# Kernel optimization log

Measured on AMD Instinct MI355X. Metric: run time of the kernel, lower is better.

The kernel has to match this reference:

```python
import jax, jax.numpy as jnp
import numpy as np

B, N, DEG = 16, 1723, 8   # batch, mesh vertices, avg degree
C, L = 512, 5             # num_channels, num_layers


def _gn(x, g, b, G):
    # GroupNorm over (B, C, N), normalize per group over (C//G, N)
    Bx, Cx, Nx = x.shape
    xr = x.reshape(Bx, G, Cx // G, Nx)
    m = xr.mean(axis=(2, 3), keepdims=True)
    v = xr.var(axis=(2, 3), keepdims=True)
    xr = (xr - m) * jax.lax.rsqrt(v + 1e-5)
    return xr.reshape(Bx, Cx, Nx) * g[None, :, None] + b[None, :, None]


def _glin(W, b, x):
    # per-vertex linear: (O,I) @ (B,I,N) + b
    return jnp.einsum('oi,bin->bon', W, x) + b[None, :, None]


def _gconv(x, W, b, src, dst, w):
    # GraphConvolution: support = x^T @ W, then sparse adjacency spmm via edge list
    sup = jnp.einsum('bcn,cd->bnd', x, W)          # (B, N, C)
    msg = sup[:, src, :] * w[None, :, None]        # gather neighbors (B, E, C)
    agg = jnp.zeros_like(sup).at[:, dst, :].add(msg) + b[None, None, :]
    return agg.transpose(0, 2, 1)                  # back to (B, C, N)


def _resblock(x, p, src, dst, w):
    (pre_g, pre_b, l1W, l1b, n1g, n1b, cW, cb, n2g, n2b, l2W, l2b, skW, skb) = p
    Cin, Ch = x.shape[1], l1W.shape[0]
    y = jax.nn.relu(_gn(x, pre_g, pre_b, Cin // 8))
    y = _glin(l1W, l1b, y)
    y = jax.nn.relu(_gn(y, n1g, n1b, Ch // 8))
    y = _gconv(y, cW, cb, src, dst, w)
    y = jax.nn.relu(_gn(y, n2g, n2b, Ch // 8))
    y = _glin(l2W, l2b, y)
    if skW is not None:
        x = _glin(skW, skb, x)
    return x + y


def setup_inputs() -> dict:
    key = jax.random.key(0)
    ks = iter(jax.random.split(key, 64))
    s = 0.02
    w = lambda shp: jax.random.normal(next(ks), shp, jnp.float32) * s
    z = lambda shp: jnp.zeros(shp, jnp.float32)
    o = lambda shp: jnp.ones(shp, jnp.float32)
    H = C // 2
    E = N * DEG
    inp = {}
    inp['image_resnet'] = jax.random.normal(next(ks), (B, 2048), jnp.float32)
    inp['ref_vertices'] = jax.random.normal(next(ks), (3, N), jnp.float32)
    inp['adj_src'] = jax.random.randint(next(ks), (E,), 0, N, jnp.int32)
    inp['adj_dst'] = jnp.repeat(jnp.arange(N, dtype=jnp.int32), DEG)
    inp['adj_w'] = jnp.full((E,), 1.0 / DEG, jnp.float32)
    inp['lin0_W'] = w((2 * C, 3 + 2048)); inp['lin0_b'] = z((2 * C,))
    inp['b0_pre_g'] = o((2 * C,)); inp['b0_pre_b'] = z((2 * C,))
    inp['b0_lin1_W'] = w((H, 2 * C)); inp['b0_lin1_b'] = z((H,))
    inp['b0_n1_g'] = o((H,)); inp['b0_n1_b'] = z((H,))
    inp['b0_conv_W'] = w((H, H)); inp['b0_conv_b'] = z((H,))
    inp['b0_n2_g'] = o((H,)); inp['b0_n2_b'] = z((H,))
    inp['b0_lin2_W'] = w((C, H)); inp['b0_lin2_b'] = z((C,))
    inp['b0_skip_W'] = w((C, 2 * C)); inp['b0_skip_b'] = z((C,))
    inp['blk_pre_g'] = o((L, C)); inp['blk_pre_b'] = z((L, C))
    inp['blk_lin1_W'] = w((L, H, C)); inp['blk_lin1_b'] = z((L, H))
    inp['blk_n1_g'] = o((L, H)); inp['blk_n1_b'] = z((L, H))
    inp['blk_conv_W'] = w((L, H, H)); inp['blk_conv_b'] = z((L, H))
    inp['blk_n2_g'] = o((L, H)); inp['blk_n2_b'] = z((L, H))
    inp['blk_lin2_W'] = w((L, C, H)); inp['blk_lin2_b'] = z((L, C))
    inp['h1_W'] = w((64, C)); inp['h1_b'] = z((64,))
    inp['h2_W'] = w((32, 64)); inp['h2_b'] = z((32,))
    inp['hn_g'] = o((32,)); inp['hn_b'] = z((32,))
    inp['h3_W'] = w((3, 32)); inp['h3_b'] = z((3,))
    return inp


def reference(image_resnet, ref_vertices, adj_src, adj_dst, adj_w,
              lin0_W, lin0_b,
              b0_pre_g, b0_pre_b, b0_lin1_W, b0_lin1_b, b0_n1_g, b0_n1_b,
              b0_conv_W, b0_conv_b, b0_n2_g, b0_n2_b, b0_lin2_W, b0_lin2_b,
              b0_skip_W, b0_skip_b,
              blk_pre_g, blk_pre_b, blk_lin1_W, blk_lin1_b, blk_n1_g, blk_n1_b,
              blk_conv_W, blk_conv_b, blk_n2_g, blk_n2_b, blk_lin2_W, blk_lin2_b,
              h1_W, h1_b, h2_W, h2_b, hn_g, hn_b, h3_W, h3_b):
    Bx, Nv = image_resnet.shape[0], ref_vertices.shape[1]
    img = jnp.broadcast_to(image_resnet[:, :, None], (Bx, 2048, Nv))
    verts = jnp.broadcast_to(ref_vertices[None], (Bx, 3, Nv))
    x = jnp.concatenate([verts, img], axis=1)                 # (B, 2051, N)
    x = _glin(lin0_W, lin0_b, x)                              # (B, 1024, N)
    x = _resblock(x, (b0_pre_g, b0_pre_b, b0_lin1_W, b0_lin1_b, b0_n1_g, b0_n1_b,
                      b0_conv_W, b0_conv_b, b0_n2_g, b0_n2_b, b0_lin2_W, b0_lin2_b,
                      b0_skip_W, b0_skip_b), adj_src, adj_dst, adj_w)  # (B, 512, N)
    for i in range(blk_pre_g.shape[0]):
        x = _resblock(x, (blk_pre_g[i], blk_pre_b[i], blk_lin1_W[i], blk_lin1_b[i],
                          blk_n1_g[i], blk_n1_b[i], blk_conv_W[i], blk_conv_b[i],
                          blk_n2_g[i], blk_n2_b[i], blk_lin2_W[i], blk_lin2_b[i],
                          None, None), adj_src, adj_dst, adj_w)
    # shape decoder head
    y = jax.nn.relu(_glin(h1_W, h1_b, x))
    y = _glin(h2_W, h2_b, y)
    y = jax.nn.relu(_gn(y, hn_g, hn_b, 4))   # GroupNorm(32//8, 32)
    y = _glin(h3_W, h3_b, y)                 # (B, 3, N)
    return y
```

## Files before the change

### kernel.cpp

```cpp
#include <hip/hip_runtime.h>
#include <cstddef>
#include <cstdint>

#define THREADS 256

typedef short bh8 __attribute__((ext_vector_type(8)));
typedef float fx4 __attribute__((ext_vector_type(4)));

__device__ __forceinline__ float bf2f(unsigned short u) {
  union { unsigned int i; float f; } x;
  x.i = ((unsigned int)u) << 16;
  return x.f;
}
__device__ __forceinline__ unsigned short f2bf(float f) {
  union { float f; unsigned int i; } x;
  x.f = f;
  unsigned int r = x.i + 0x7fffu + ((x.i >> 16) & 1u);
  return (unsigned short)(r >> 16);
}

__device__ __forceinline__ void gld16(const void* g, void* l) {
  __builtin_amdgcn_global_load_lds(
      (const __attribute__((address_space(1))) unsigned int*)g,
      (__attribute__((address_space(3))) unsigned int*)l, 16, 0, 0);
}

__global__ __launch_bounds__(THREADS) void transpose_img_k(
    const float* __restrict__ img, float* __restrict__ imgT) {
  int gid = blockIdx.x * THREADS + threadIdx.x;
  if (gid >= 2048 * 16) return;
  int k = gid >> 4, b = gid & 15;
  imgT[k * 16 + b] = img[b * 2048 + k];
}

__global__ __launch_bounds__(THREADS) void pack_wv_k(
    const float* __restrict__ W, float* __restrict__ wv) {
  int gid = blockIdx.x * THREADS + threadIdx.x;
  if (gid >= 3 * 1024) return;
  int k = gid >> 10, c = gid & 1023;
  wv[gid] = W[(size_t)c * 2051 + k];
}

__global__ __launch_bounds__(THREADS) void vertproj_k(
    const float* __restrict__ wv, const float* __restrict__ verts,
    float* __restrict__ v, int N) {
  int gid = blockIdx.x * THREADS + threadIdx.x;
  int c = gid & 1023, n = gid >> 10;
  if (n >= N) return;
  v[(size_t)n * 1024 + c] =
      wv[c] * verts[n] + wv[1024 + c] * verts[N + n] + wv[2048 + c] * verts[2 * N + n];
}

__global__ __launch_bounds__(THREADS) void ugemm2_k(
    const float* __restrict__ W, int ldw, int woff,
    const float* __restrict__ bias, const float* __restrict__ X,
    float* __restrict__ out, int K, int Ofull, int xl, int ks) {
  int tid = threadIdx.x;
  int b = tid & 15, cl = tid >> 4;
  int c = blockIdx.x * 16 + cl;
  int k0 = blockIdx.y * ks, k1 = k0 + ks;
  const float* wr = W + woff + (size_t)c * ldw;
  float a0 = 0.f, a1 = 0.f;
  if (xl) {
    const float* xr = X + (size_t)b * K;
    for (int k = k0; k < k1; k += 2) {
      a0 = fmaf(wr[k], xr[k], a0);
      a1 = fmaf(wr[k + 1], xr[k + 1], a1);
    }
  } else {
    for (int k = k0; k < k1; k += 2) {
      a0 = fmaf(wr[k], X[k * 16 + b], a0);
      a1 = fmaf(wr[k + 1], X[(k + 1) * 16 + b], a1);
    }
  }
  float r = a0 + a1;
  if (blockIdx.y == 0) r += bias[c];
  atomicAdd(&out[(size_t)b * Ofull + c], r);
}

struct PackDesc {
  const float* W;
  unsigned short* out;
  int O, K, TW, nOt;
  unsigned cum;
};
struct PackArgs {
  PackDesc d[8];
  unsigned grand;
};

__global__ __launch_bounds__(THREADS) void packall_k(PackArgs a) {
  unsigned gid = blockIdx.x * THREADS + threadIdx.x;
  if (gid >= a.grand) return;
  int s = 0;
#pragma unroll
  for (int i = 1; i < 8; ++i)
    if (gid >= a.d[i].cum) s = i;
#pragma unroll
  for (int i = 0; i < 8; ++i) {
    if (s != i) continue;
    const float* W = a.d[i].W;
    int O = a.d[i].O, K = a.d[i].K, TW = a.d[i].TW, nOt = a.d[i].nOt;
    unsigned e = gid - a.d[i].cum;
    int j = (int)(e & 7);
    int m = (int)((e >> 3) & 127);
    unsigned rest = e >> 10;
    int K8 = K >> 3;
    int kg = (int)(rest % (unsigned)K8);
    unsigned rest2 = rest / (unsigned)K8;
    int ot = (int)(rest2 % (unsigned)nOt);
    int l = (int)(rest2 / (unsigned)nOt);
    int o = ot * 128 + m, k = kg * 8 + j;
    float val = 0.f;
    if (o < O)
      val = TW ? W[(size_t)l * O * K + (size_t)k * O + o]
               : W[(size_t)l * O * K + (size_t)o * K + k];
    a.d[i].out[e] = f2bf(val);
  }
}

__global__ __launch_bounds__(THREADS) void vstats_k(
    const float* __restrict__ v, float* __restrict__ sv,
    float* __restrict__ sq, int N) {
  int c = blockIdx.x * THREADS + threadIdx.x;
  float s = 0.f, q = 0.f;
  for (int n = blockIdx.y; n < N; n += 16) {
    float x = v[(size_t)n * 1024 + c];
    s += x; q += x * x;
  }
  atomicAdd(&sv[c], s);
  atomicAdd(&sq[c], q);
}

__global__ __launch_bounds__(THREADS) void combine_b0_k(
    const float* __restrict__ ub, const float* __restrict__ sv,
    const float* __restrict__ sq, float* __restrict__ mean,
    float* __restrict__ rinv, int N) {
  int bg = blockIdx.x * THREADS + threadIdx.x;
  if (bg >= 2048) return;
  int b = bg >> 7, g = bg & 127;
  int c0 = g * 8;
  float fN = (float)N;
  float s = 0.f, q = 0.f;
#pragma unroll
  for (int j = 0; j < 8; ++j) {
    float u = ub[b * 1024 + c0 + j];
    float svc = sv[c0 + j];
    s += fN * u + svc;
    q += fN * u * u + 2.f * u * svc + sq[c0 + j];
  }
  float inv = 1.f / (8.f * fN);
  float m = s * inv;
  float var = q * inv - m * m;
  mean[bg] = m;
  rinv[bg] = rsqrtf(var + 1e-5f);
}

__global__ __launch_bounds__(THREADS) void agg16_k(
    const unsigned short* __restrict__ Xn, const float* __restrict__ sarr,
    const float* __restrict__ qarr, const float* __restrict__ gamma,
    const float* __restrict__ beta, const int* __restrict__ src,
    const float* __restrict__ wgt, unsigned short* __restrict__ outb, int N,
    int NPn) {
  int w = threadIdx.x >> 6, lane = threadIdx.x & 63;
  int n = blockIdx.x * 4 + w;
  if (n >= N) return;
  int b = blockIdx.y;
  int c = lane * 4;
  int g = c >> 3;
  float sfac = 1.f / (8.f * (float)N);
  float svv = sarr[b * 32 + g], qv = qarr[b * 32 + g];
  float m = svv * sfac;
  float ri = rsqrtf(qv * sfac - m * m + 1e-5f);
  float4 g4 = *(const float4*)(gamma + c);
  float4 b4 = *(const float4*)(beta + c);
  const int* sp = src + n * 8;
  const float* wp = wgt + n * 8;
  const unsigned short* base = Xn + (size_t)b * NPn * 256;
  float a0 = 0.f, a1 = 0.f, a2 = 0.f, a3 = 0.f;
#pragma unroll
  for (int j = 0; j < 8; ++j) {
    int sidx = sp[j];
    float wj = wp[j];
    ushort4 x4 = *(const ushort4*)(base + (size_t)sidx * 256 + c);
    a0 = fmaf(wj, fmaxf((bf2f(x4.x) - m) * ri * g4.x + b4.x, 0.f), a0);
    a1 = fmaf(wj, fmaxf((bf2f(x4.y) - m) * ri * g4.y + b4.y, 0.f), a1);
    a2 = fmaf(wj, fmaxf((bf2f(x4.z) - m) * ri * g4.z + b4.z, 0.f), a2);
    a3 = fmaf(wj, fmaxf((bf2f(x4.w) - m) * ri * g4.w + b4.w, 0.f), a3);
  }
  ushort4 h;
  h.x = f2bf(a0); h.y = f2bf(a1); h.z = f2bf(a2); h.w = f2bf(a3);
  *(ushort4*)(outb + ((size_t)b * NPn + n) * 256 + c) = h;
}

template <int XM, int RES, int OUT16, int ORELU, int STATS>
__global__ __launch_bounds__(THREADS) void mgemm_k(
    const unsigned short* __restrict__ Wp, const float* __restrict__ bias,
    const void* __restrict__ Xv, const float* __restrict__ ub,
    const float* __restrict__ vv, const float* __restrict__ meanS,
    const float* __restrict__ rinvS, const float* __restrict__ gamma,
    const float* __restrict__ beta, const float* __restrict__ resA,
    const float* __restrict__ resB, float* __restrict__ sacc,
    float* __restrict__ qacc, void* __restrict__ outv, int O, int I, int N,
    int NPn) {
  constexpr int BBUF = (XM == 4) ? 2 : 1;
  __shared__ unsigned short Alds[2][4][128][8];
  __shared__ unsigned short Blds[BBUF][4][128][8];
  const int tid = threadIdx.x;
  const int lane = tid & 63;
  const int wid = tid >> 6;
  const int wm = wid & 1, wn = wid >> 1;
  const int n0 = blockIdx.x * 128;
  const int o0 = blockIdx.y * 128;
  const int b = blockIdx.z;
  const int K8 = I >> 3;
  const unsigned short* wp = Wp + (size_t)blockIdx.y * K8 * 1024;

  fx4 acc[4][4];
#pragma unroll
  for (int i = 0; i < 4; ++i)
#pragma unroll
    for (int j = 0; j < 4; ++j) {
      acc[i][j][0] = 0.f; acc[i][j][1] = 0.f;
      acc[i][j][2] = 0.f; acc[i][j][3] = 0.f;
    }

  const int sko = tid >> 6;
  const int sn = (tid & 63) * 2;
  const int mlane = lane & 15;
  const int klane = lane >> 4;

  auto dmaA = [&](int k0, int buf) {
    const unsigned short* asrc = wp + (size_t)(k0 >> 3) * 1024;
    unsigned short* ab = &Alds[buf][0][0][0];
    gld16(asrc + (size_t)tid * 8, ab + (size_t)tid * 8);
    gld16(asrc + (size_t)(tid + 256) * 8, ab + (size_t)(tid + 256) * 8);
  };
  auto dmaB4 = [&](int k0, int buf) {
    const unsigned short* xs =
        (const unsigned short*)Xv + ((size_t)b * NPn + n0) * I + k0 + wid * 8;
    unsigned short* bb = &Blds[buf][0][0][0] + (size_t)wid * 1024;
    gld16(xs + (size_t)lane * I, bb + (size_t)lane * 8);
    gld16(xs + (size_t)(lane + 64) * I, bb + 512 + (size_t)lane * 8);
  };

  uint4 br0, br1;
  float4 f00, f01, f10, f11, u01, u23;

  auto gloadB = [&](int k0) {
    const int ke = k0 + sko * 8;
    if (XM == 3) {
      const unsigned short* p =
          (const unsigned short*)Xv + ((size_t)b * NPn + n0 + sn) * I + ke;
      br0 = *(const uint4*)p;
      br1 = *(const uint4*)(p + I);
    } else if (XM == 1) {
      const float* p = vv + (size_t)(n0 + sn) * I + ke;
      f00 = *(const float4*)p;       f01 = *(const float4*)(p + 4);
      f10 = *(const float4*)(p + I); f11 = *(const float4*)(p + I + 4);
      const float* up = ub + (size_t)b * I + ke;
      u01 = *(const float4*)up;
      u23 = *(const float4*)(up + 4);
    } else if (XM == 0 || XM == 2) {
      const float* p = (const float*)Xv + ((size_t)b * NPn + n0 + sn) * I + ke;
      f00 = *(const float4*)p;       f01 = *(const float4*)(p + 4);
      f10 = *(const float4*)(p + I); f11 = *(const float4*)(p + I + 4);
    }
  };

  union H8 { unsigned short u[8]; uint4 q; };

  auto bstoreB = [&](int k0) {
    const int ke = k0 + sko * 8;
    float x0[8], x1[8];
    if (XM == 3) {
      H8 hr0, hr1;
      hr0.q = br0; hr1.q = br1;
#pragma unroll
      for (int j = 0; j < 8; ++j) {
        x0[j] = bf2f(hr0.u[j]);
        x1[j] = bf2f(hr1.u[j]);
      }
    } else {
      x0[0] = f00.x; x0[1] = f00.y; x0[2] = f00.z; x0[3] = f00.w;
      x0[4] = f01.x; x0[5] = f01.y; x0[6] = f01.z; x0[7] = f01.w;
      x1[0] = f10.x; x1[1] = f10.y; x1[2] = f10.z; x1[3] = f10.w;
      x1[4] = f11.x; x1[5] = f11.y; x1[6] = f11.z; x1[7] = f11.w;
    }
    if (XM == 1) {
      float uu[8] = {u01.x, u01.y, u01.z, u01.w, u23.x, u23.y, u23.z, u23.w};
#pragma unroll
      for (int j = 0; j < 8; ++j) { x0[j] += uu[j]; x1[j] += uu[j]; }
    }
    if (XM != 0) {
      float m_, r_;
      if (XM == 1) {
        m_ = meanS[b * K8 + (ke >> 3)];
        r_ = rinvS[b * K8 + (ke >> 3)];
      } else {
        float sfac = 1.f / (8.f * (float)N);
        float sv = meanS[b * K8 + (ke >> 3)];
        float qv = rinvS[b * K8 + (ke >> 3)];
        m_ = sv * sfac;
        r_ = rsqrtf(qv * sfac - m_ * m_ + 1e-5f);
      }
      float4 g0 = *(const float4*)(gamma + ke);
      float4 g1 = *(const float4*)(gamma + ke + 4);
      float4 e0 = *(const float4*)(beta + ke);
      float4 e1 = *(const float4*)(beta + ke + 4);
      float ga[8] = {g0.x, g0.y, g0.z, g0.w, g1.x, g1.y, g1.z, g1.w};
      float bb[8] = {e0.x, e0.y, e0.z, e0.w, e1.x, e1.y, e1.z, e1.w};
#pragma unroll
      for (int j = 0; j < 8; ++j) {
        x0[j] = fmaxf((x0[j] - m_) * r_ * ga[j] + bb[j], 0.f);
        x1[j] = fmaxf((x1[j] - m_) * r_ * ga[j] + bb[j], 0.f);
      }
    }
    H8 h0, h1;
#pragma unroll
    for (int j = 0; j < 8; ++j) {
      h0.u[j] = f2bf(x0[j]);
      h1.u[j] = f2bf(x1[j]);
    }
    *(uint4*)&Blds[0][sko][sn][0] = h0.q;
    *(uint4*)&Blds[0][sko][sn + 1][0] = h1.q;
  };

  auto compute = [&](int ab, int bb) {
    bh8 af[4], bfr[4];
#pragma unroll
    for (int mi = 0; mi < 4; ++mi)
      af[mi] = *(const bh8*)(&Alds[ab][klane][wm * 64 + mi * 16 + mlane][0]);
#pragma unroll
    for (int ni = 0; ni < 4; ++ni)
      bfr[ni] = *(const bh8*)(&Blds[bb][klane][wn * 64 + ni * 16 + mlane][0]);
#pragma unroll
    for (int mi = 0; mi < 4; ++mi)
#pragma unroll
      for (int ni = 0; ni < 4; ++ni)
        acc[mi][ni] = __builtin_amdgcn_mfma_f32_16x16x32_bf16(
            af[mi], bfr[ni], acc[mi][ni], 0, 0, 0);
  };

  if (XM == 4) {
    dmaA(0, 0);
    dmaB4(0, 0);
    __syncthreads();
    for (int k0 = 0; k0 < I; k0 += 32) {
      const int cur = (k0 >> 5) & 1;
      if (k0 + 32 < I) {
        dmaA(k0 + 32, cur ^ 1);
        dmaB4(k0 + 32, cur ^ 1);
      }
      compute(cur, cur);
      __syncthreads();
    }
  } else {
    dmaA(0, 0);
    gloadB(0);
    for (int k0 = 0; k0 < I; k0 += 32) {
      const int cur = (k0 >> 5) & 1;
      bstoreB(k0);
      __syncthreads();
      if (k0 + 32 < I) {
        dmaA(k0 + 32, cur ^ 1);
        gloadB(k0 + 32);
      }
      compute(cur, 0);
      __syncthreads();
    }
  }

  float sred[4] = {0.f, 0.f, 0.f, 0.f};
  float qred[4] = {0.f, 0.f, 0.f, 0.f};
#pragma unroll
  for (int mi = 0; mi < 4; ++mi) {
    const int o = o0 + wm * 64 + mi * 16 + klane * 4;
    if (o >= O) continue;
    float4 bi;
    if (bias) bi = *(const float4*)(bias + o);
    float4 ra;
    if (RES == 2) ra = *(const float4*)(resA + (size_t)b * O + o);
#pragma unroll
    for (int ni = 0; ni < 4; ++ni) {
      const int n = n0 + wn * 64 + ni * 16 + mlane;
      if (n >= N) continue;
      float v0 = acc[mi][ni][0], v1 = acc[mi][ni][1];
      float v2 = acc[mi][ni][2], v3 = acc[mi][ni][3];
      if (bias) { v0 += bi.x; v1 += bi.y; v2 += bi.z; v3 += bi.w; }
      size_t obase = ((size_t)b * NPn + n) * O + o;
      if (RES == 1) {
        float4 rv = *(const float4*)(resA + obase);
        v0 += rv.x; v1 += rv.y; v2 += rv.z; v3 += rv.w;
      }
      if (RES == 2) {
        float4 rb = *(const float4*)(resB + (size_t)n * O + o);
        v0 += ra.x + rb.x; v1 += ra.y + rb.y;
        v2 += ra.z + rb.z; v3 += ra.w + rb.w;
      }
      if (ORELU) {
        v0 = fmaxf(v0, 0.f); v1 = fmaxf(v1, 0.f);
        v2 = fmaxf(v2, 0.f); v3 = fmaxf(v3, 0.f);
      }
      if (STATS) {
        sred[mi] += v0 + v1 + v2 + v3;
        qred[mi] += v0 * v0 + v1 * v1 + v2 * v2 + v3 * v3;
      }
      if (OUT16) {
        ushort4 h;
        h.x = f2bf(v0); h.y = f2bf(v1); h.z = f2bf(v2); h.w = f2bf(v3);
        *(ushort4*)((unsigned short*)outv + obase) = h;
      } else {
        float4 fv; fv.x = v0; fv.y = v1; fv.z = v2; fv.w = v3;
        *(float4*)((float*)outv + obase) = fv;
      }
    }
  }
  if (STATS) {
    const int G = O >> 3;
#pragma unroll
    for (int mi = 0; mi < 4; ++mi) {
      const int o = o0 + wm * 64 + mi * 16 + klane * 4;
      if (o >= O) continue;
      float s = sred[mi], q = qred[mi];
#pragma unroll
      for (int m = 1; m < 16; m <<= 1) {
        s += __shfl_xor(s, m, 64);
        q += __shfl_xor(q, m, 64);
      }
      if (mlane == 0) {
        atomicAdd(&sacc[b * G + (o >> 3)], s);
        atomicAdd(&qacc[b * G + (o >> 3)], q);
      }
    }
  }
}

__global__ __launch_bounds__(THREADS) void h2_k(
    const float* __restrict__ t64, const float* __restrict__ W,
    const float* __restrict__ bias, float* __restrict__ out, int N, int NPn) {
  int gid = blockIdx.x * THREADS + threadIdx.x;
  int o = gid & 31, n = gid >> 5;
  if (n >= N) return;
  int b = blockIdx.y;
  const float* xr = t64 + ((size_t)b * NPn + n) * 64;
  const float* wr = W + o * 64;
  float acc = bias[o];
#pragma unroll
  for (int i = 0; i < 64; i += 4) {
    float4 w4 = *(const float4*)(wr + i);
    float4 x4 = *(const float4*)(xr + i);
    acc += w4.x * x4.x + w4.y * x4.y + w4.z * x4.z + w4.w * x4.w;
  }
  out[((size_t)b * NPn + n) * 32 + o] = acc;
}

__global__ __launch_bounds__(THREADS) void stats_head_k(
    const float* __restrict__ X, float* __restrict__ mean,
    float* __restrict__ rinv, int NPn, int N) {
  int b = blockIdx.x >> 2, g = blockIdx.x & 3;
  int c = g * 8 + (threadIdx.x & 7);
  float s = 0.f, q = 0.f;
  for (int n = threadIdx.x >> 3; n < N; n += 32) {
    float x = X[((size_t)b * NPn + n) * 32 + c];
    s += x; q += x * x;
  }
#pragma unroll
  for (int off = 32; off; off >>= 1) {
    s += __shfl_down(s, off, 64);
    q += __shfl_down(q, off, 64);
  }
  __shared__ float shs[4], shq[4];
  int wv = threadIdx.x >> 6;
  if ((threadIdx.x & 63) == 0) { shs[wv] = s; shq[wv] = q; }
  __syncthreads();
  if (threadIdx.x == 0) {
    s = shs[0] + shs[1] + shs[2] + shs[3];
    q = shq[0] + shq[1] + shq[2] + shq[3];
    float inv = 1.f / (8.f * (float)N);
    float m = s * inv;
    float var = q * inv - m * m;
    mean[blockIdx.x] = m;
    rinv[blockIdx.x] = rsqrtf(var + 1e-5f);
  }
}

__global__ __launch_bounds__(THREADS) void h3_k(
    const float* __restrict__ t32, const float* __restrict__ mean,
    const float* __restrict__ rinv, const float* __restrict__ g,
    const float* __restrict__ be, const float* __restrict__ W,
    const float* __restrict__ bias, float* __restrict__ out, int N, int NPn) {
  int n = blockIdx.x * THREADS + threadIdx.x;
  if (n >= N) return;
  int b = blockIdx.y;
  const float* xr = t32 + ((size_t)b * NPn + n) * 32;
  float y0 = bias[0], y1 = bias[1], y2 = bias[2];
#pragma unroll
  for (int c = 0; c < 32; ++c) {
    float m = mean[b * 4 + (c >> 3)], ri = rinv[b * 4 + (c >> 3)];
    float x = fmaxf((xr[c] - m) * ri * g[c] + be[c], 0.f);
    y0 = fmaf(W[c], x, y0);
    y1 = fmaf(W[32 + c], x, y1);
    y2 = fmaf(W[64 + c], x, y2);
  }
  out[(size_t)b * 3 * N + n] = y0;
  out[(size_t)b * 3 * N + N + n] = y1;
  out[(size_t)b * 3 * N + 2 * N + n] = y2;
}

extern "C" void kernel_launch(void* const* d_in, const int* in_sizes, int n_in,
                              void* d_out, int out_size, void* d_ws,
                              size_t ws_size, hipStream_t stream) {
  (void)n_in; (void)out_size; (void)ws_size;
  const float* img = (const float*)d_in[0];
  const float* verts = (const float*)d_in[1];
  const int* src = (const int*)d_in[2];
  const float* adjw = (const float*)d_in[4];
  const float* lin0_W = (const float*)d_in[5];
  const float* lin0_b = (const float*)d_in[6];
  const float* b0_pre_g = (const float*)d_in[7];
  const float* b0_pre_b = (const float*)d_in[8];
  const float* b0_lin1_W = (const float*)d_in[9];
  const float* b0_lin1_b = (const float*)d_in[10];
  const float* b0_n1_g = (const float*)d_in[11];
  const float* b0_n1_b = (const float*)d_in[12];
  const float* b0_conv_W = (const float*)d_in[13];
  const float* b0_conv_b = (const float*)d_in[14];
  const float* b0_n2_g = (const float*)d_in[15];
  const float* b0_n2_b = (const float*)d_in[16];
  const float* b0_lin2_W = (const float*)d_in[17];
  const float* b0_lin2_b = (const float*)d_in[18];
  const float* b0_skip_W = (const float*)d_in[19];
  const float* b0_skip_b = (const float*)d_in[20];
  const float* blk_pre_g = (const float*)d_in[21];
  const float* blk_pre_b = (const float*)d_in[22];
  const float* blk_lin1_W = (const float*)d_in[23];
  const float* blk_lin1_b = (const float*)d_in[24];
  const float* blk_n1_g = (const float*)d_in[25];
  const float* blk_n1_b = (const float*)d_in[26];
  const float* blk_conv_W = (const float*)d_in[27];
  const float* blk_conv_b = (const float*)d_in[28];
  const float* blk_n2_g = (const float*)d_in[29];
  const float* blk_n2_b = (const float*)d_in[30];
  const float* blk_lin2_W = (const float*)d_in[31];
  const float* blk_lin2_b = (const float*)d_in[32];
  const float* h1_W = (const float*)d_in[33];
  const float* h1_b = (const float*)d_in[34];
  const float* h2_W = (const float*)d_in[35];
  const float* h2_b = (const float*)d_in[36];
  const float* hn_g = (const float*)d_in[37];
  const float* hn_b = (const float*)d_in[38];
  const float* h3_W = (const float*)d_in[39];
  const float* h3_b = (const float*)d_in[40];

  const int N = in_sizes[1] / 3;
  const int NP = ((N + 127) / 128) * 128;
  const int NT128 = NP / 128;
  const int B = 16;

  char* wsb = (char*)d_ws;
  size_t off = 0;
  auto alloc = [&](size_t nbytes) {
    void* p = wsb + off;
    off += (nbytes + 255) & ~(size_t)255;
    return p;
  };
  float* xbuf = (float*)alloc((size_t)B * NP * 512 * 4);
  unsigned short* t256a = (unsigned short*)alloc((size_t)B * NP * 256 * 2);
  unsigned short* t256b = (unsigned short*)alloc((size_t)B * NP * 256 * 2);
  float* vbuf = (float*)alloc((size_t)NP * 1024 * 4);
  float* svbuf = (float*)alloc((size_t)NP * 512 * 4);
  float* t64 = (float*)alloc((size_t)B * NP * 64 * 4);
  float* t32 = (float*)alloc((size_t)B * NP * 32 * 4);
  float* imgT = (float*)alloc(2048 * 16 * 4);
  float* wv = (float*)alloc(3 * 1024 * 4);
  float* m0 = (float*)alloc(2048 * 4);
  float* r0 = (float*)alloc(2048 * 4);
  float* mh = (float*)alloc(64 * 4);
  float* rh = (float*)alloc(64 * 4);
  float* zerobuf = (float*)alloc((size_t)49152 * 4);
  float* sA = zerobuf;
  float* qA = zerobuf + 11264;
  float* sv = zerobuf + 22528;
  float* sq = zerobuf + 23552;
  float* ub = zerobuf + 24576;
  float* suT = zerobuf + 40960;
  const int off_b0n1 = 0, off_b0n2 = 512;
  auto off_pre = [](int l) { return 1024 + l * 2048; };
  auto off_n1 = [](int l) { return 1024 + l * 2048 + 1024; };
  auto off_n2 = [](int l) { return 1024 + l * 2048 + 1536; };
  unsigned short* pw_b0l1 = (unsigned short*)alloc(262144 * 2);
  unsigned short* pw_b0cv = (unsigned short*)alloc(65536 * 2);
  unsigned short* pw_b0l2 = (unsigned short*)alloc(131072 * 2);
  unsigned short* pw_b0sk = (unsigned short*)alloc(524288 * 2);
  unsigned short* pw_l1 = (unsigned short*)alloc(655360 * 2);
  unsigned short* pw_cv = (unsigned short*)alloc(327680 * 2);
  unsigned short* pw_l2 = (unsigned short*)alloc(655360 * 2);
  unsigned short* pw_h1 = (unsigned short*)alloc(65536 * 2);

  dim3 blk(THREADS);
  auto cdiv = [](size_t a, size_t b) { return (unsigned)((a + b - 1) / b); };

  hipMemsetAsync(zerobuf, 0, (size_t)49152 * 4, stream);

  {
    PackArgs pa;
    unsigned c = 0;
    auto set = [&](int i, const float* W, unsigned short* o, int O, int K,
                   int TW, int nOt, unsigned tot) {
      pa.d[i] = {W, o, O, K, TW, nOt, c};
      c += tot;
    };
    set(0, b0_lin1_W, pw_b0l1, 256, 1024, 0, 2, 262144);
    set(1, b0_conv_W, pw_b0cv, 256, 256, 1, 2, 65536);
    set(2, b0_lin2_W, pw_b0l2, 512, 256, 0, 4, 131072);
    set(3, b0_skip_W, pw_b0sk, 512, 1024, 0, 4, 524288);
    set(4, blk_lin1_W, pw_l1, 256, 512, 0, 2, 655360);
    set(5, blk_conv_W, pw_cv, 256, 256, 1, 2, 327680);
    set(6, blk_lin2_W, pw_l2, 512, 256, 0, 4, 655360);
    set(7, h1_W, pw_h1, 64, 512, 0, 1, 65536);
    pa.grand = c;
    packall_k<<<cdiv(pa.grand, THREADS), blk, 0, stream>>>(pa);
  }

  transpose_img_k<<<cdiv(2048 * 16, THREADS), blk, 0, stream>>>(img, imgT);
  pack_wv_k<<<cdiv(3072, THREADS), blk, 0, stream>>>(lin0_W, wv);
  ugemm2_k<<<dim3(64, 16), blk, 0, stream>>>(lin0_W, 2051, 3, lin0_b, imgT,
                                             ub, 2048, 1024, 0, 128);
  vertproj_k<<<cdiv((size_t)N * 1024, THREADS), blk, 0, stream>>>(wv, verts, vbuf, N);

  const dim3 aggGrid(cdiv(N, 4), 16);

  vstats_k<<<dim3(4, 16), blk, 0, stream>>>(vbuf, sv, sq, N);
  combine_b0_k<<<dim3(8), blk, 0, stream>>>(ub, sv, sq, m0, r0, N);
  mgemm_k<1, 0, 1, 0, 1><<<dim3(NT128, 2, 16), blk, 0, stream>>>(
      pw_b0l1, b0_lin1_b, nullptr, ub, vbuf, m0, r0, b0_pre_g, b0_pre_b,
      nullptr, nullptr, sA + off_b0n1, qA + off_b0n1, t256a, 256, 1024, N, NP);
  ugemm2_k<<<dim3(32, 8), blk, 0, stream>>>(b0_skip_W, 1024, 0, b0_skip_b, ub,
                                            suT, 1024, 512, 1, 128);
  mgemm_k<0, 0, 0, 0, 0><<<dim3(NT128, 4, 1), blk, 0, stream>>>(
      pw_b0sk, nullptr, vbuf, nullptr, nullptr, nullptr, nullptr, nullptr,
      nullptr, nullptr, nullptr, nullptr, nullptr, svbuf, 512, 1024, N, NP);
  agg16_k<<<aggGrid, blk, 0, stream>>>(t256a, sA + off_b0n1, qA + off_b0n1,
                                       b0_n1_g, b0_n1_b, src, adjw, t256b, N, NP);
  mgemm_k<4, 0, 1, 0, 1><<<dim3(NT128, 2, 16), blk, 0, stream>>>(
      pw_b0cv, b0_conv_b, t256b, nullptr, nullptr, nullptr, nullptr, nullptr,
      nullptr, nullptr, nullptr, sA + off_b0n2, qA + off_b0n2, t256a, 256, 256, N, NP);
  mgemm_k<3, 2, 0, 0, 1><<<dim3(NT128, 4, 16), blk, 0, stream>>>(
      pw_b0l2, b0_lin2_b, t256a, nullptr, nullptr, sA + off_b0n2, qA + off_b0n2,
      b0_n2_g, b0_n2_b, suT, svbuf, sA + off_pre(0), qA + off_pre(0), xbuf,
      512, 256, N, NP);

  for (int l = 0; l < 5; ++l) {
    const float* pg = blk_pre_g + l * 512;
    const float* pb = blk_pre_b + l * 512;
    const unsigned short* l1W = pw_l1 + (size_t)l * 131072;
    const float* l1b = blk_lin1_b + l * 256;
    const float* n1g = blk_n1_g + l * 256;
    const float* n1b = blk_n1_b + l * 256;
    const unsigned short* cW = pw_cv + (size_t)l * 65536;
    const float* cb = blk_conv_b + l * 256;
    const float* n2g = blk_n2_g + l * 256;
    const float* n2b = blk_n2_b + l * 256;
    const unsigned short* l2W = pw_l2 + (size_t)l * 131072;
    const float* l2b = blk_lin2_b + l * 512;

    mgemm_k<2, 0, 1, 0, 1><<<dim3(NT128, 2, 16), blk, 0, stream>>>(
        l1W, l1b, xbuf, nullptr, nullptr, sA + off_pre(l), qA + off_pre(l), pg,
        pb, nullptr, nullptr, sA + off_n1(l), qA + off_n1(l), t256a, 256, 512, N, NP);
    agg16_k<<<aggGrid, blk, 0, stream>>>(t256a, sA + off_n1(l), qA + off_n1(l),
                                         n1g, n1b, src, adjw, t256b, N, NP);
    mgemm_k<4, 0, 1, 0, 1><<<dim3(NT128, 2, 16), blk, 0, stream>>>(
        cW, cb, t256b, nullptr, nullptr, nullptr, nullptr, nullptr, nullptr,
        nullptr, nullptr, sA + off_n2(l), qA + off_n2(l), t256a, 256, 256, N, NP);
    if (l < 4) {
      mgemm_k<3, 1, 0, 0, 1><<<dim3(NT128, 4, 16), blk, 0, stream>>>(
          l2W, l2b, t256a, nullptr, nullptr, sA + off_n2(l), qA + off_n2(l),
          n2g, n2b, xbuf, nullptr, sA + off_pre(l + 1), qA + off_pre(l + 1),
          xbuf, 512, 256, N, NP);
    } else {
      mgemm_k<3, 1, 0, 0, 0><<<dim3(NT128, 4, 16), blk, 0, stream>>>(
          l2W, l2b, t256a, nullptr, nullptr, sA + off_n2(l), qA + off_n2(l),
          n2g, n2b, xbuf, nullptr, nullptr, nullptr, xbuf, 512, 256, N, NP);
    }
  }

  mgemm_k<0, 0, 0, 1, 0><<<dim3(NT128, 1, 16), blk, 0, stream>>>(
      pw_h1, h1_b, xbuf, nullptr, nullptr, nullptr, nullptr, nullptr, nullptr,
      nullptr, nullptr, nullptr, nullptr, t64, 64, 512, N, NP);
  h2_k<<<dim3(cdiv((size_t)N * 32, THREADS), 16), blk, 0, stream>>>(
      t64, h2_W, h2_b, t32, N, NP);
  stats_head_k<<<dim3(64), blk, 0, stream>>>(t32, mh, rh, NP, N);
  h3_k<<<dim3(cdiv(N, THREADS), 16), blk, 0, stream>>>(
      t32, mh, rh, hn_g, hn_b, h3_W, h3_b, (float*)d_out, N, NP);
}
```

Baseline: 1.401 ms.

## Fuse neighbor aggregation into conv GEMM B-load and keep bf16 residual copy

Removes the standalone agg16 kernel and folds the GroupNorm+ReLU+weighted 8-neighbor gather into a new XM==5 B-tile loader of the graph-conv GEMM. It saves one launch and one intermediate write/read per block. Separately, the lin2 GEMM now also writes a bf16 copy of the residual stream (DUAL), so the next lin1 GEMM reads bf16 instead of fp32. The cost is more registers and gather latency inside the GEMM's B staging, which may lower occupancy or stall the MFMA pipeline. There is also an extra store and extra memory for the bf16 copy.

```diff
diff --git a/kernel.cpp b/kernel.cpp
--- a/kernel.cpp
+++ b/kernel.cpp
@@ -156,53 +156,17 @@
   rinv[bg] = rsqrtf(var + 1e-5f);
 }
 
-__global__ __launch_bounds__(THREADS) void agg16_k(
-    const unsigned short* __restrict__ Xn, const float* __restrict__ sarr,
-    const float* __restrict__ qarr, const float* __restrict__ gamma,
-    const float* __restrict__ beta, const int* __restrict__ src,
-    const float* __restrict__ wgt, unsigned short* __restrict__ outb, int N,
-    int NPn) {
-  int w = threadIdx.x >> 6, lane = threadIdx.x & 63;
-  int n = blockIdx.x * 4 + w;
-  if (n >= N) return;
-  int b = blockIdx.y;
-  int c = lane * 4;
-  int g = c >> 3;
-  float sfac = 1.f / (8.f * (float)N);
-  float svv = sarr[b * 32 + g], qv = qarr[b * 32 + g];
-  float m = svv * sfac;
-  float ri = rsqrtf(qv * sfac - m * m + 1e-5f);
-  float4 g4 = *(const float4*)(gamma + c);
-  float4 b4 = *(const float4*)(beta + c);
-  const int* sp = src + n * 8;
-  const float* wp = wgt + n * 8;
-  const unsigned short* base = Xn + (size_t)b * NPn * 256;
-  float a0 = 0.f, a1 = 0.f, a2 = 0.f, a3 = 0.f;
-#pragma unroll
-  for (int j = 0; j < 8; ++j) {
-    int sidx = sp[j];
-    float wj = wp[j];
-    ushort4 x4 = *(const ushort4*)(base + (size_t)sidx * 256 + c);
-    a0 = fmaf(wj, fmaxf((bf2f(x4.x) - m) * ri * g4.x + b4.x, 0.f), a0);
-    a1 = fmaf(wj, fmaxf((bf2f(x4.y) - m) * ri * g4.y + b4.y, 0.f), a1);
-    a2 = fmaf(wj, fmaxf((bf2f(x4.z) - m) * ri * g4.z + b4.z, 0.f), a2);
-    a3 = fmaf(wj, fmaxf((bf2f(x4.w) - m) * ri * g4.w + b4.w, 0.f), a3);
-  }
-  ushort4 h;
-  h.x = f2bf(a0); h.y = f2bf(a1); h.z = f2bf(a2); h.w = f2bf(a3);
-  *(ushort4*)(outb + ((size_t)b * NPn + n) * 256 + c) = h;
-}
-
-template <int XM, int RES, int OUT16, int ORELU, int STATS>
+template <int XM, int RES, int OUT16, int ORELU, int STATS, int DUAL>
 __global__ __launch_bounds__(THREADS) void mgemm_k(
     const unsigned short* __restrict__ Wp, const float* __restrict__ bias,
     const void* __restrict__ Xv, const float* __restrict__ ub,
     const float* __restrict__ vv, const float* __restrict__ meanS,
     const float* __restrict__ rinvS, const float* __restrict__ gamma,
     const float* __restrict__ beta, const float* __restrict__ resA,
-    const float* __restrict__ resB, float* __restrict__ sacc,
-    float* __restrict__ qacc, void* __restrict__ outv, int O, int I, int N,
-    int NPn) {
+    const float* __restrict__ resB, const int* __restrict__ srcp,
+    const float* __restrict__ wgtp, float* __restrict__ sacc,
+    float* __restrict__ qacc, void* __restrict__ outv,
+    void* __restrict__ outv2, int O, int I, int N, int NPn) {
   constexpr int BBUF = (XM == 4) ? 2 : 1;
   __shared__ unsigned short Alds[2][4][128][8];
   __shared__ unsigned short Blds[BBUF][4][128][8];
@@ -246,6 +210,24 @@
 
   uint4 br0, br1;
   float4 f00, f01, f10, f11, u01, u23;
+  int go0[8], go1[8];
+  float gw0[8], gw1[8];
+  uint4 g0[8], g1[8];
+  if (XM == 5) {
+    int nc0 = n0 + sn; if (nc0 >= N) nc0 = N - 1;
+    int nc1 = n0 + sn + 1; if (nc1 >= N) nc1 = N - 1;
+    const int* sp0 = srcp + nc0 * 8;
+    const int* sp1 = srcp + nc1 * 8;
+    const float* wp0 = wgtp + nc0 * 8;
+    const float* wp1 = wgtp + nc1 * 8;
+#pragma unroll
+    for (int e = 0; e < 8; ++e) {
+      go0[e] = sp0[e] * I;
+      go1[e] = sp1[e] * I;
+      gw0[e] = wp0[e];
+      gw1[e] = wp1[e];
+    }
+  }
 
   auto gloadB = [&](int k0) {
     const int ke = k0 + sko * 8;
@@ -254,6 +236,14 @@
           (const unsigned short*)Xv + ((size_t)b * NPn + n0 + sn) * I + ke;
       br0 = *(const uint4*)p;
       br1 = *(const uint4*)(p + I);
+    } else if (XM == 5) {
+      const unsigned short* xb =
+          (const unsigned short*)Xv + (size_t)b * NPn * I + ke;
+#pragma unroll
+      for (int e = 0; e < 8; ++e) {
+        g0[e] = *(const uint4*)(xb + (size_t)go0[e]);
+        g1[e] = *(const uint4*)(xb + (size_t)go1[e]);
+      }
     } else if (XM == 1) {
       const float* p = vv + (size_t)(n0 + sn) * I + ke;
       f00 = *(const float4*)p;       f01 = *(const float4*)(p + 4);
@@ -273,6 +263,46 @@
   auto bstoreB = [&](int k0) {
     const int ke = k0 + sko * 8;
     float x0[8], x1[8];
+    if (XM == 5) {
+      float sfac = 1.f / (8.f * (float)N);
+      float sv = meanS[b * K8 + (ke >> 3)];
+      float qv = rinvS[b * K8 + (ke >> 3)];
+      float m_ = sv * sfac;
+      float r_ = rsqrtf(qv * sfac - m_ * m_ + 1e-5f);
+      float4 gq0 = *(const float4*)(gamma + ke);
+      float4 gq1 = *(const float4*)(gamma + ke + 4);
+      float4 eq0 = *(const float4*)(beta + ke);
+      float4 eq1 = *(const float4*)(beta + ke + 4);
+      float A[8] = {gq0.x, gq0.y, gq0.z, gq0.w, gq1.x, gq1.y, gq1.z, gq1.w};
+      float C[8] = {eq0.x, eq0.y, eq0.z, eq0.w, eq1.x, eq1.y, eq1.z, eq1.w};
+#pragma unroll
+      for (int j = 0; j < 8; ++j) {
+        A[j] *= r_;
+        C[j] -= m_ * A[j];
+        x0[j] = 0.f;
+        x1[j] = 0.f;
+      }
+#pragma unroll
+      for (int e = 0; e < 8; ++e) {
+        H8 h0c, h1c;
+        h0c.q = g0[e]; h1c.q = g1[e];
+        float w0 = gw0[e], w1 = gw1[e];
+#pragma unroll
+        for (int j = 0; j < 8; ++j) {
+          x0[j] = fmaf(w0, fmaxf(fmaf(bf2f(h0c.u[j]), A[j], C[j]), 0.f), x0[j]);
+          x1[j] = fmaf(w1, fmaxf(fmaf(bf2f(h1c.u[j]), A[j], C[j]), 0.f), x1[j]);
+        }
+      }
+      H8 h0, h1;
+#pragma unroll
+      for (int j = 0; j < 8; ++j) {
+        h0.u[j] = f2bf(x0[j]);
+        h1.u[j] = f2bf(x1[j]);
+      }
+      *(uint4*)&Blds[0][sko][sn][0] = h0.q;
+      *(uint4*)&Blds[0][sko][sn + 1][0] = h1.q;
+      return;
+    }
     if (XM == 3) {
       H8 hr0, hr1;
       hr0.q = br0; hr1.q = br1;
@@ -304,12 +334,12 @@
         m_ = sv * sfac;
         r_ = rsqrtf(qv * sfac - m_ * m_ + 1e-5f);
       }
-      float4 g0 = *(const float4*)(gamma + ke);
-      float4 g1 = *(const float4*)(gamma + ke + 4);
-      float4 e0 = *(const float4*)(beta + ke);
-      float4 e1 = *(const float4*)(beta + ke + 4);
-      float ga[8] = {g0.x, g0.y, g0.z, g0.w, g1.x, g1.y, g1.z, g1.w};
-      float bb[8] = {e0.x, e0.y, e0.z, e0.w, e1.x, e1.y, e1.z, e1.w};
+      float4 g0q = *(const float4*)(gamma + ke);
+      float4 g1q = *(const float4*)(gamma + ke + 4);
+      float4 e0q = *(const float4*)(beta + ke);
+      float4 e1q = *(const float4*)(beta + ke + 4);
+      float ga[8] = {g0q.x, g0q.y, g0q.z, g0q.w, g1q.x, g1q.y, g1q.z, g1q.w};
+      float bb[8] = {e0q.x, e0q.y, e0q.z, e0q.w, e1q.x, e1q.y, e1q.z, e1q.w};
 #pragma unroll
       for (int j = 0; j < 8; ++j) {
         x0[j] = fmaxf((x0[j] - m_) * r_ * ga[j] + bb[j], 0.f);
@@ -413,6 +443,11 @@
       } else {
         float4 fv; fv.x = v0; fv.y = v1; fv.z = v2; fv.w = v3;
         *(float4*)((float*)outv + obase) = fv;
+      }
+      if (DUAL) {
+        ushort4 hh;
+        hh.x = f2bf(v0); hh.y = f2bf(v1); hh.z = f2bf(v2); hh.w = f2bf(v3);
+        *(ushort4*)((unsigned short*)outv2 + obase) = hh;
       }
     }
   }
@@ -566,6 +601,7 @@
     return p;
   };
   float* xbuf = (float*)alloc((size_t)B * NP * 512 * 4);
+  unsigned short* xb16 = (unsigned short*)alloc((size_t)B * NP * 512 * 2);
   unsigned short* t256a = (unsigned short*)alloc((size_t)B * NP * 256 * 2);
   unsigned short* t256b = (unsigned short*)alloc((size_t)B * NP * 256 * 2);
   float* vbuf = (float*)alloc((size_t)NP * 1024 * 4);
@@ -629,27 +665,26 @@
                                              ub, 2048, 1024, 0, 128);
   vertproj_k<<<cdiv((size_t)N * 1024, THREADS), blk, 0, stream>>>(wv, verts, vbuf, N);
 
-  const dim3 aggGrid(cdiv(N, 4), 16);
-
   vstats_k<<<dim3(4, 16), blk, 0, stream>>>(vbuf, sv, sq, N);
   combine_b0_k<<<dim3(8), blk, 0, stream>>>(ub, sv, sq, m0, r0, N);
-  mgemm_k<1, 0, 1, 0, 1><<<dim3(NT128, 2, 16), blk, 0, stream>>>(
+  mgemm_k<1, 0, 1, 0, 1, 0><<<dim3(NT128, 2, 16), blk, 0, stream>>>(
       pw_b0l1, b0_lin1_b, nullptr, ub, vbuf, m0, r0, b0_pre_g, b0_pre_b,
-      nullptr, nullptr, sA + off_b0n1, qA + off_b0n1, t256a, 256, 1024, N, NP);
+      nullptr, nullptr, nullptr, nullptr, sA + off_b0n1, qA + off_b0n1, t256a,
+      nullptr, 256, 1024, N, NP);
   ugemm2_k<<<dim3(32, 8), blk, 0, stream>>>(b0_skip_W, 1024, 0, b0_skip_b, ub,
                                             suT, 1024, 512, 1, 128);
-  mgemm_k<0, 0, 0, 0, 0><<<dim3(NT128, 4, 1), blk, 0, stream>>>(
+  mgemm_k<0, 0, 0, 0, 0, 0><<<dim3(NT128, 4, 1), blk, 0, stream>>>(
       pw_b0sk, nullptr, vbuf, nullptr, nullptr, nullptr, nullptr, nullptr,
-      nullptr, nullptr, nullptr, nullptr, nullptr, svbuf, 512, 1024, N, NP);
-  agg16_k<<<aggGrid, blk, 0, stream>>>(t256a, sA + off_b0n1, qA + off_b0n1,
-                                       b0_n1_g, b0_n1_b, src, adjw, t256b, N, NP);
-  mgemm_k<4, 0, 1, 0, 1><<<dim3(NT128, 2, 16), blk, 0, stream>>>(
-      pw_b0cv, b0_conv_b, t256b, nullptr, nullptr, nullptr, nullptr, nullptr,
-      nullptr, nullptr, nullptr, sA + off_b0n2, qA + off_b0n2, t256a, 256, 256, N, NP);
-  mgemm_k<3, 2, 0, 0, 1><<<dim3(NT128, 4, 16), blk, 0, stream>>>(
-      pw_b0l2, b0_lin2_b, t256a, nullptr, nullptr, sA + off_b0n2, qA + off_b0n2,
-      b0_n2_g, b0_n2_b, suT, svbuf, sA + off_pre(0), qA + off_pre(0), xbuf,
-      512, 256, N, NP);
+      nullptr, nullptr, nullptr, nullptr, nullptr, nullptr, nullptr, svbuf,
+      nullptr, 512, 1024, N, NP);
+  mgemm_k<5, 0, 1, 0, 1, 0><<<dim3(NT128, 2, 16), blk, 0, stream>>>(
+      pw_b0cv, b0_conv_b, t256a, nullptr, nullptr, sA + off_b0n1,
+      qA + off_b0n1, b0_n1_g, b0_n1_b, nullptr, nullptr, src, adjw,
+      sA + off_b0n2, qA + off_b0n2, t256b, nullptr, 256, 256, N, NP);
+  mgemm_k<3, 2, 0, 0, 1, 1><<<dim3(NT128, 4, 16), blk, 0, stream>>>(
+      pw_b0l2, b0_lin2_b, t256b, nullptr, nullptr, sA + off_b0n2,
+      qA + off_b0n2, b0_n2_g, b0_n2_b, suT, svbuf, nullptr, nullptr,
+      sA + off_pre(0), qA + off_pre(0), xbuf, xb16, 512, 256, N, NP);
 
   for (int l = 0; l < 5; ++l) {
     const float* pg = blk_pre_g + l * 512;
@@ -665,29 +700,31 @@
     const unsigned short* l2W = pw_l2 + (size_t)l * 131072;
     const float* l2b = blk_lin2_b + l * 512;
 
-    mgemm_k<2, 0, 1, 0, 1><<<dim3(NT128, 2, 16), blk, 0, stream>>>(
-        l1W, l1b, xbuf, nullptr, nullptr, sA + off_pre(l), qA + off_pre(l), pg,
-        pb, nullptr, nullptr, sA + off_n1(l), qA + off_n1(l), t256a, 256, 512, N, NP);
-    agg16_k<<<aggGrid, blk, 0, stream>>>(t256a, sA + off_n1(l), qA + off_n1(l),
-                                         n1g, n1b, src, adjw, t256b, N, NP);
-    mgemm_k<4, 0, 1, 0, 1><<<dim3(NT128, 2, 16), blk, 0, stream>>>(
-        cW, cb, t256b, nullptr, nullptr, nullptr, nullptr, nullptr, nullptr,
-        nullptr, nullptr, sA + off_n2(l), qA + off_n2(l), t256a, 256, 256, N, NP);
+    mgemm_k<3, 0, 1, 0, 1, 0><<<dim3(NT128, 2, 16), blk, 0, stream>>>(
+        l1W, l1b, xb16, nullptr, nullptr, sA + off_pre(l), qA + off_pre(l), pg,
+        pb, nullptr, nullptr, nullptr, nullptr, sA + off_n1(l), qA + off_n1(l),
+        t256a, nullptr, 256, 512, N, NP);
+    mgemm_k<5, 0, 1, 0, 1, 0><<<dim3(NT128, 2, 16), blk, 0, stream>>>(
+        cW, cb, t256a, nullptr, nullptr, sA + off_n1(l), qA + off_n1(l), n1g,
+        n1b, nullptr, nullptr, src, adjw, sA + off_n2(l), qA + off_n2(l),
+        t256b, nullptr, 256, 256, N, NP);
     if (l < 4) {
-      mgemm_k<3, 1, 0, 0, 1><<<dim3(NT128, 4, 16), blk, 0, stream>>>(
-          l2W, l2b, t256a, nullptr, nullptr, sA + off_n2(l), qA + off_n2(l),
-          n2g, n2b, xbuf, nullptr, sA + off_pre(l + 1), qA + off_pre(l + 1),
-          xbuf, 512, 256, N, NP);
+      mgemm_k<3, 1, 0, 0, 1, 1><<<dim3(NT128, 4, 16), blk, 0, stream>>>(
+          l2W, l2b, t256b, nullptr, nullptr, sA + off_n2(l), qA + off_n2(l),
+          n2g, n2b, xbuf, nullptr, nullptr, nullptr, sA + off_pre(l + 1),
+          qA + off_pre(l + 1), xbuf, xb16, 512, 256, N, NP);
     } else {
-      mgemm_k<3, 1, 0, 0, 0><<<dim3(NT128, 4, 16), blk, 0, stream>>>(
-          l2W, l2b, t256a, nullptr, nullptr, sA + off_n2(l), qA + off_n2(l),
-          n2g, n2b, xbuf, nullptr, nullptr, nullptr, xbuf, 512, 256, N, NP);
-    }
-  }
-
-  mgemm_k<0, 0, 0, 1, 0><<<dim3(NT128, 1, 16), blk, 0, stream>>>(
+      mgemm_k<3, 1, 0, 0, 0, 0><<<dim3(NT128, 4, 16), blk, 0, stream>>>(
+          l2W, l2b, t256b, nullptr, nullptr, sA + off_n2(l), qA + off_n2(l),
+          n2g, n2b, xbuf, nullptr, nullptr, nullptr, nullptr, nullptr, xbuf,
+          nullptr, 512, 256, N, NP);
+    }
+  }
+
+  mgemm_k<0, 0, 0, 1, 0, 0><<<dim3(NT128, 1, 16), blk, 0, stream>>>(
       pw_h1, h1_b, xbuf, nullptr, nullptr, nullptr, nullptr, nullptr, nullptr,
-      nullptr, nullptr, nullptr, nullptr, t64, 64, 512, N, NP);
+      nullptr, nullptr, nullptr, nullptr, nullptr, nullptr, t64, nullptr, 64,
+      512, N, NP);
   h2_k<<<dim3(cdiv((size_t)N * 32, THREADS), 16), blk, 0, stream>>>(
       t64, h2_W, h2_b, t32, N, NP);
   stats_head_k<<<dim3(64), blk, 0, stream>>>(t32, mh, rh, NP, N);
```

Result: slower. 1.752 ms (+25.1%).
